# Optimization experiments

Measured on AMD Instinct MI355X. Metric: run time of the kernel, lower is better.

## Reference

```python
import jax, jax.numpy as jnp
import numpy as np

B, O, C, HID, H, W = 4, 8, 256, 128, 64, 64
STEPS = 2  # message passing steps


def _conv3x3(x, w, b):
    # x: [N,Cin,H,W], w: [Cout,Cin,3,3]
    y = jax.lax.conv_general_dilated(x, w, window_strides=(1, 1), padding='SAME',
                                     dimension_numbers=('NCHW', 'OIHW', 'NCHW'))
    return y + b[None, :, None, None]


def setup_inputs() -> dict:
    key = jax.random.key(0)
    ks = jax.random.split(key, 6)
    return {
        'batch_node_feats': jax.random.normal(ks[0], (B, C, H, W), jnp.float32),
        'batch_previous_masks': jax.random.uniform(ks[1], (B, O, H, W), jnp.float32),
        'batch_valid_indices': jnp.ones((B, O), jnp.bool_),
        'batch_previous_states': jnp.zeros((B, O), jnp.float32),  # unused (use_temporal_features=False)
        'enc_w': jax.random.normal(ks[2], (HID, C + 1, 3, 3), jnp.float32) * 0.02,
        'enc_b': jnp.zeros((HID,), jnp.float32),
        'gcn_w': jax.random.normal(ks[3], (HID, 2 * HID, 3, 3), jnp.float32) * 0.02,
        'gcn_b': jnp.zeros((HID,), jnp.float32),
        'ro_w': jax.random.normal(ks[4], (1, C + HID, 3, 3), jnp.float32) * 0.02,
        'ro_b': jnp.zeros((1,), jnp.float32),
    }


def reference(batch_node_feats, batch_previous_masks, batch_valid_indices,
              batch_previous_states, enc_w, enc_b, gcn_w, gcn_b, ro_w, ro_b):
    # All objects valid (batch_valid_indices all True) -> fully vectorized over B and O.
    feats = jnp.broadcast_to(batch_node_feats[:, None], (B, O, C, H, W))
    # Mask encoder: per-object state from frame feats + previous object mask.
    enc_in = jnp.concatenate([feats, batch_previous_masks[:, :, None]], axis=2)
    states = jax.nn.relu(_conv3x3(enc_in.reshape(B * O, C + 1, H, W), enc_w, enc_b))
    states = states.reshape(B, O, HID, H, W)
    # Fully-connected message passing: neighbors of i = all objects except i.
    for _ in range(STEPS):
        agg = states.sum(axis=1, keepdims=True) - states  # sum over others
        gcn_in = jnp.concatenate([states, agg], axis=2).reshape(B * O, 2 * HID, H, W)
        states = jax.nn.relu(_conv3x3(gcn_in, gcn_w, gcn_b)).reshape(B, O, HID, H, W)
    # Readout: per-object mask logits -> sigmoid.
    ro_in = jnp.concatenate([feats, states], axis=2).reshape(B * O, C + HID, H, W)
    out_masks = jax.nn.sigmoid(_conv3x3(ro_in, ro_w, ro_b)).reshape(B, O, H, W)
    return out_masks  # out_states is None when use_temporal_features=False
```

## Files before the change

### kernel.cpp

```cpp
#include <hip/hip_runtime.h>
#include <math.h>


typedef unsigned short ushort_t;
typedef _Float16 f16x8 __attribute__((ext_vector_type(8)));
typedef float f32x4 __attribute__((ext_vector_type(4)));

#define GLDS(gsrc, ldst)                                                      \
    __builtin_amdgcn_global_load_lds(                                         \
        (const __attribute__((address_space(1))) unsigned int*)(gsrc),        \
        (__attribute__((address_space(3))) unsigned int*)(ldst), 16, 0, 0)

__device__ __forceinline__ ushort_t f2h(float f) {
    _Float16 h = (_Float16)f;
    return *(ushort_t*)&h;
}
__device__ __forceinline__ float h2f(ushort_t u) {
    _Float16 h = *(_Float16*)&u;
    return (float)h;
}
__device__ __forceinline__ int swz(int p, int q) {
    return q ^ (((p >> 1) + (p >> 3)) & 3);
}

__global__ __launch_bounds__(256) void prep_weights(
    const float* __restrict__ enc_w, const float* __restrict__ gcn_w,
    const float* __restrict__ ro_w,
    ushort_t* __restrict__ WencF, ushort_t* __restrict__ WgcnS,
    ushort_t* __restrict__ WgcnD, ushort_t* __restrict__ WroQ,
    ushort_t* __restrict__ WroS)
{
    int i = blockIdx.x * 256 + threadIdx.x;
    if (i < 294912) {
        int u8 = i & 7, q = (i >> 3) & 3, co = (i >> 5) & 127, tc = i >> 12;
        int t = tc >> 3, cc = tc & 7;
        int ci = cc * 32 + swz(co & 63, q) * 8 + u8;
        WencF[i] = f2h(enc_w[(co * 257 + ci) * 9 + t]);
    } else if (i < 442368) {
        int j = i - 294912;
        int u8 = j & 7, q = (j >> 3) & 3, co = (j >> 5) & 127, tc = j >> 12;
        int t = tc >> 2, cc = tc & 3;
        int ci = cc * 32 + swz(co & 63, q) * 8 + u8;
        WgcnS[j] = f2h(gcn_w[(co * 256 + 128 + ci) * 9 + t]);
    } else if (i < 589824) {
        int j = i - 442368;
        int u8 = j & 7, q = (j >> 3) & 3, co = (j >> 5) & 127, tc = j >> 12;
        int t = tc >> 2, cc = tc & 3;
        int ci = cc * 32 + swz(co & 63, q) * 8 + u8;
        WgcnD[j] = f2h(gcn_w[(co * 256 + ci) * 9 + t] - gcn_w[(co * 256 + 128 + ci) * 9 + t]);
    } else if (i < 592128) {
        int j = i - 589824;
        int k = j & 7, r = j >> 3;
        int t = r % 9, cq = r / 9, q = cq & 3, cc = cq >> 2;
        WroQ[j] = f2h(ro_w[(cc * 32 + q * 8 + k) * 9 + t]);
    } else if (i < 593280) {
        int j = i - 592128;
        int k = j & 7, r = j >> 3;
        int t = r % 9, cq = r / 9, q = cq & 3, cc = cq >> 2;
        WroS[j] = f2h(ro_w[(256 + cc * 32 + q * 8 + k) * 9 + t]);
    }
}

__global__ __launch_bounds__(256) void feats_to_hwc(const float* __restrict__ feats,
                                                    ushort_t* __restrict__ featsT)
{
    __shared__ float tile[64][65];
    int img = blockIdx.z, ct = blockIdx.y, pt = blockIdx.x;
    int t = threadIdx.x;
    int px_l = t & 63;
    const float* src = feats + ((size_t)img * 256 + ct * 64) * 4096 + pt * 64;
#pragma unroll
    for (int j = 0; j < 16; ++j) {
        int ci_l = (t >> 6) + j * 4;
        tile[px_l][ci_l] = src[(size_t)ci_l * 4096 + px_l];
    }
    __syncthreads();
    int px = t >> 2;
#pragma unroll
    for (int j = 0; j < 2; ++j) {
        int c8 = ((t & 3) + j * 4) * 8;
        uint4 v; ushort_t* pv = (ushort_t*)&v;
#pragma unroll
        for (int k = 0; k < 8; ++k) pv[k] = f2h(tile[px][c8 + k]);
        int cc = ct * 2 + (c8 >> 5);
        int q = (c8 & 31) >> 3;
        *(uint4*)(featsT + ((size_t)img * 8 + cc) * 131072 +
                  (size_t)(pt * 64 + px) * 32 + swz(px, q) * 8) = v;
    }
}

__global__ __launch_bounds__(256, 3) void conv_mfma(
    const ushort_t* __restrict__ xA, const ushort_t* __restrict__ WA,
    ushort_t* __restrict__ outA, int nA,
    const ushort_t* __restrict__ xB, const ushort_t* __restrict__ WB,
    float* __restrict__ outB, int nB,
    int ncc_img, int ncc_blk)
{
    __shared__ ushort_t raw[25088];
    ushort_t* xs = raw;
    ushort_t* wlds = raw + 16896;
    ushort_t* eb16 = raw;
    float* eb32 = (float*)raw;

    const int rp = blockIdx.x, img = blockIdx.y, kz = blockIdx.z;
    const int row0 = rp * 2;
    const int cc0 = kz * ncc_blk;
    const int nchunk = 9 * ncc_blk;
    const int tid = threadIdx.x;
    const int w = tid >> 6, lane = tid & 63, lq = lane >> 4, lr = lane & 15;
    const int cg = w >> 1, pg = w & 1;

    const bool isA = img < nA;
    const ushort_t* x = isA ? xA + (size_t)img * ncc_img * 131072
                            : xB + (size_t)(img - nA) * ncc_img * 131072;
    const ushort_t* W = isA ? WA : WB;

    int aoff[4], boff[3][4];
#pragma unroll
    for (int cf = 0; cf < 4; ++cf) {
        int co = cg * 64 + cf * 16 + lr;
        aoff[cf] = co * 32 + swz(co & 63, lq) * 8;
    }
#pragma unroll
    for (int dx = 0; dx < 3; ++dx)
#pragma unroll
        for (int p = 0; p < 4; ++p) {
            int col = dx + lr + p * 16;
            boff[dx][p] = col * 32 + swz((col - 1) & 63, lq) * 8;
        }

    if (tid < 64) {
        int b = tid >> 5, r = (tid >> 3) & 3, c = (tid >> 2) & 1, s = tid & 3;
        *(uint4*)(xs + b * 8448 + r * 2112 + (c ? 65 : 0) * 32 + s * 8) =
            make_uint4(0, 0, 0, 0);
    }

    f32x4 acc[4][4];
#pragma unroll
    for (int a = 0; a < 4; ++a)
#pragma unroll
        for (int p = 0; p < 4; ++p) acc[a][p] = (f32x4){0.f, 0.f, 0.f, 0.f};

    const int gy = row0 - 1 + w;
    const bool row_ok = (unsigned)gy < 64u;
#define STAGE_ACT(cc_, buf_)                                                    \
    {                                                                           \
        ushort_t* dst = xs + (buf_) * 8448 + w * 2112 + 32;                     \
        if (row_ok) {                                                           \
            const ushort_t* src = x + (size_t)(cc_) * 131072 + (size_t)gy * 2048; \
            GLDS(src + 0 * 512 + lane * 8, dst + 0 * 512);                      \
            GLDS(src + 1 * 512 + lane * 8, dst + 1 * 512);                      \
            GLDS(src + 2 * 512 + lane * 8, dst + 2 * 512);                      \
            GLDS(src + 3 * 512 + lane * 8, dst + 3 * 512);                      \
        } else {                                                                \
            *(uint4*)(dst + 0 * 512 + lane * 8) = make_uint4(0, 0, 0, 0);       \
            *(uint4*)(dst + 1 * 512 + lane * 8) = make_uint4(0, 0, 0, 0);       \
            *(uint4*)(dst + 2 * 512 + lane * 8) = make_uint4(0, 0, 0, 0);       \
            *(uint4*)(dst + 3 * 512 + lane * 8) = make_uint4(0, 0, 0, 0);       \
        }                                                                       \
    }
#define STAGE_W(t_, cc_, buf_)                                                  \
    {                                                                           \
        const ushort_t* src = W + ((size_t)((t_) * ncc_img + (cc_)) * 4096);    \
        ushort_t* dst = wlds + (buf_) * 4096;                                   \
        GLDS(src + (w * 2 + 0) * 512 + lane * 8, dst + (w * 2 + 0) * 512);      \
        GLDS(src + (w * 2 + 1) * 512 + lane * 8, dst + (w * 2 + 1) * 512);      \
    }

    STAGE_ACT(cc0, 0);
    STAGE_W(0, cc0, 0);

    int kc = 0;
    for (int ccl = 0; ccl < ncc_blk; ++ccl) {
        const int cc = cc0 + ccl;
        const int xb = ccl & 1;
#pragma unroll
        for (int t = 0; t < 9; ++t, ++kc) {
            __syncthreads();
            if (kc + 1 < nchunk) {
                if (t == 8) {
                    STAGE_W(0, cc + 1, (kc + 1) & 1);
                    STAGE_ACT(cc + 1, (ccl + 1) & 1);
                } else {
                    STAGE_W(t + 1, cc, (kc + 1) & 1);
                }
            }
            const int dy = t / 3, dx = t - 3 * dy;
            const ushort_t* wl = wlds + (kc & 1) * 4096;
            const ushort_t* xl = xs + xb * 8448 + (pg + dy) * 2112;
            f16x8 A0 = *(const f16x8*)(wl + aoff[0]);
            f16x8 A1 = *(const f16x8*)(wl + aoff[1]);
            f16x8 A2 = *(const f16x8*)(wl + aoff[2]);
            f16x8 A3 = *(const f16x8*)(wl + aoff[3]);
#pragma unroll
            for (int p = 0; p < 4; ++p) {
                f16x8 Bf = *(const f16x8*)(xl + boff[dx][p]);
                acc[0][p] = __builtin_amdgcn_mfma_f32_16x16x32_f16(A0, Bf, acc[0][p], 0, 0, 0);
                acc[1][p] = __builtin_amdgcn_mfma_f32_16x16x32_f16(A1, Bf, acc[1][p], 0, 0, 0);
                acc[2][p] = __builtin_amdgcn_mfma_f32_16x16x32_f16(A2, Bf, acc[2][p], 0, 0, 0);
                acc[3][p] = __builtin_amdgcn_mfma_f32_16x16x32_f16(A3, Bf, acc[3][p], 0, 0, 0);
            }
        }
    }

    if (isA) {
        ushort_t* obase = outA + (size_t)img * ncc_img * 131072;
#pragma unroll
        for (int r = 0; r < 2; ++r) {
            __syncthreads();
            if (pg == r) {
#pragma unroll
                for (int cf = 0; cf < 4; ++cf)
#pragma unroll
                    for (int pf = 0; pf < 4; ++pf) {
                        int px = pf * 16 + lr;
                        int co_l = cg * 64 + cf * 16 + lq * 4;
                        ushort_t pk[4];
#pragma unroll
                        for (int j = 0; j < 4; ++j) pk[j] = f2h(acc[cf][pf][j]);
                        *(uint2*)(eb16 + px * 136 + co_l) = *(uint2*)pk;
                    }
            }
            __syncthreads();
#pragma unroll
            for (int k = 0; k < 4; ++k) {
                int i = tid + k * 256;
                int px = i >> 4, c16 = i & 15;
                uint4 v = *(uint4*)(eb16 + px * 136 + c16 * 8);
                *(uint4*)(obase + (size_t)(c16 >> 2) * 131072 +
                          (size_t)((row0 + r) * 64 + px) * 32 + swz(px, c16 & 3) * 8) = v;
            }
        }
    } else {
        float* obase = outB + ((size_t)kz * nB + (img - nA)) * 524288;
#pragma unroll
        for (int r = 0; r < 2; ++r)
#pragma unroll
            for (int h = 0; h < 2; ++h) {
                __syncthreads();
                if (pg == r && cg == h) {
#pragma unroll
                    for (int cf = 0; cf < 4; ++cf)
#pragma unroll
                        for (int pf = 0; pf < 4; ++pf)
                            *(f32x4*)(eb32 + (pf * 16 + lr) * 68 + cf * 16 + lq * 4) =
                                acc[cf][pf];
                }
                __syncthreads();
                for (int i = tid; i < 512; i += 256) {
                    int px = i >> 3, cl = (i & 7) * 8;
                    f32x4 v0 = *(f32x4*)(eb32 + px * 68 + cl);
                    f32x4 v1 = *(f32x4*)(eb32 + px * 68 + cl + 4);
                    float* op = obase + (size_t)((row0 + r) * 64 + px) * 128 + h * 64 + cl;
                    *(f32x4*)op = v0;
                    *(f32x4*)(op + 4) = v1;
                }
            }
    }
#undef STAGE_ACT
#undef STAGE_W
}

__global__ __launch_bounds__(256) void combine_sum(
    ushort_t* __restrict__ S, const float* __restrict__ U2,
    const float* __restrict__ gcn_b, ushort_t* __restrict__ USum)
{
    int i = blockIdx.x * 256 + threadIdx.x;
    int c8 = i & 15, px = (i >> 4) & 4095, b = i >> 16;
    int co = c8 * 8;
    size_t coff = (size_t)(c8 >> 2) * 131072 + (size_t)px * 32 + swz(px & 63, c8 & 3) * 8;
    const float* u = U2 + ((size_t)b * 4096 + px) * 128 + co;
    float base[8];
#pragma unroll
    for (int k = 0; k < 8; ++k) base[k] = u[k] + gcn_b[co + k];
    float s[8] = {0, 0, 0, 0, 0, 0, 0, 0};
#pragma unroll
    for (int o = 0; o < 8; ++o) {
        ushort_t* p = S + (size_t)(b * 8 + o) * 524288 + coff;
        uint4 v = *(uint4*)p;
        ushort_t* vp = (ushort_t*)&v;
        uint4 sv; ushort_t* sp = (ushort_t*)&sv;
#pragma unroll
        for (int k = 0; k < 8; ++k) {
            float f = fmaxf(h2f(vp[k]) + base[k], 0.f);
            s[k] += f;
            sp[k] = f2h(f);
        }
        *(uint4*)p = sv;
    }
    uint4 sv; ushort_t* sp = (ushort_t*)&sv;
#pragma unroll
    for (int k = 0; k < 8; ++k) sp[k] = f2h(s[k]);
    *(uint4*)(USum + (size_t)b * 524288 + coff) = sv;
}

__global__ __launch_bounds__(256) void enc_obj_sum(
    const float* __restrict__ masks, const float* __restrict__ enc_w,
    const float* __restrict__ enc_b, const float* __restrict__ U1p,
    ushort_t* __restrict__ S, ushort_t* __restrict__ USum)
{
    int i = blockIdx.x * 256 + threadIdx.x;
    int c8 = i & 15, px = (i >> 4) & 4095, b = i >> 16;
    int co = c8 * 8;
    int y = px >> 6, xx = px & 63;
    size_t coff = (size_t)(c8 >> 2) * 131072 + (size_t)px * 32 + swz(px & 63, c8 & 3) * 8;
    const float* p0 = U1p + ((size_t)b * 4096 + px) * 128 + co;
    float base[8];
#pragma unroll
    for (int k = 0; k < 8; ++k)
        base[k] = ((p0[k] + p0[k + 2097152]) + (p0[k + 4194304] + p0[k + 6291456]))
                  + enc_b[co + k];
    float wm[8][9];
#pragma unroll
    for (int k = 0; k < 8; ++k) {
        const float* wp = enc_w + (size_t)((co + k) * 257 + 256) * 9;
#pragma unroll
        for (int t = 0; t < 9; ++t) wm[k][t] = wp[t];
    }
    float s[8] = {0, 0, 0, 0, 0, 0, 0, 0};
#pragma unroll
    for (int o = 0; o < 8; ++o) {
        const float* m = masks + (size_t)(b * 8 + o) * 4096;
        float mt[9];
#pragma unroll
        for (int dy = 0; dy < 3; ++dy)
#pragma unroll
            for (int dx = 0; dx < 3; ++dx) {
                int gy_ = y + dy - 1, gx = xx + dx - 1;
                mt[dy * 3 + dx] =
                    ((unsigned)gy_ < 64u && (unsigned)gx < 64u) ? m[gy_ * 64 + gx] : 0.f;
            }
        uint4 sv; ushort_t* sp = (ushort_t*)&sv;
#pragma unroll
        for (int k = 0; k < 8; ++k) {
            float acc = base[k];
#pragma unroll
            for (int t = 0; t < 9; ++t) acc = fmaf(mt[t], wm[k][t], acc);
            acc = fmaxf(acc, 0.f);
            s[k] += acc;
            sp[k] = f2h(acc);
        }
        *(uint4*)(S + (size_t)(b * 8 + o) * 524288 + coff) = sv;
    }
    uint4 sv; ushort_t* sp = (ushort_t*)&sv;
#pragma unroll
    for (int k = 0; k < 8; ++k) sp[k] = f2h(s[k]);
    *(uint4*)(USum + (size_t)b * 524288 + coff) = sv;
}

__global__ __launch_bounds__(256) void ro_shared(
    const ushort_t* __restrict__ featsT, const ushort_t* __restrict__ WroQ,
    float* __restrict__ YR)
{
    int i = blockIdx.x * 256 + threadIdx.x;
    int cu = i & 31, px = (i >> 5) & 4095, b = i >> 17;
    int cc = cu >> 2, q = cu & 3;
    int y = px >> 6, xcol = px & 63;
    const ushort_t* wp = WroQ + (size_t)(cc * 4 + q) * 72;
    float wreg[9][8];
#pragma unroll
    for (int t = 0; t < 9; ++t) {
        uint4 wv = *(const uint4*)(wp + t * 8);
        const ushort_t* wq = (const ushort_t*)&wv;
#pragma unroll
        for (int k = 0; k < 8; ++k) wreg[t][k] = h2f(wq[k]);
    }
    const ushort_t* fb = featsT + (size_t)(b * 8 + cc) * 131072;
    float acc = 0.f;
#pragma unroll
    for (int dy = 0; dy < 3; ++dy) {
        int gy = y + dy - 1;
        if ((unsigned)gy >= 64u) continue;
#pragma unroll
        for (int dx = 0; dx < 3; ++dx) {
            int gx = xcol + dx - 1;
            if ((unsigned)gx >= 64u) continue;
            uint4 v = *(const uint4*)(fb + (size_t)(gy * 64 + gx) * 32 + swz(gx, q) * 8);
            const ushort_t* vp = (const ushort_t*)&v;
#pragma unroll
            for (int k = 0; k < 8; ++k)
                acc = fmaf(h2f(vp[k]), wreg[dy * 3 + dx][k], acc);
        }
    }
#pragma unroll
    for (int d = 16; d >= 1; d >>= 1) acc += __shfl_down(acc, d, 32);
    if (cu == 0) YR[b * 4096 + px] = acc;
}

__global__ __launch_bounds__(256) void ro_obj(
    const ushort_t* __restrict__ S, const ushort_t* __restrict__ WroS,
    const float* __restrict__ ro_b, const float* __restrict__ YR,
    float* __restrict__ out)
{
    int i = blockIdx.x * 256 + threadIdx.x;
    int cu = i & 15, px = (i >> 4) & 4095, n = i >> 16;
    int b = n >> 3;
    int cc = cu >> 2, q = cu & 3;
    int y = px >> 6, xcol = px & 63;
    const ushort_t* wp = WroS + (size_t)(cc * 4 + q) * 72;
    float wreg[9][8];
#pragma unroll
    for (int t = 0; t < 9; ++t) {
        uint4 wv = *(const uint4*)(wp + t * 8);
        const ushort_t* wq = (const ushort_t*)&wv;
#pragma unroll
        for (int k = 0; k < 8; ++k) wreg[t][k] = h2f(wq[k]);
    }
    const ushort_t* sb = S + ((size_t)n * 4 + cc) * 131072;
    float acc = 0.f;
#pragma unroll
    for (int dy = 0; dy < 3; ++dy) {
        int gy = y + dy - 1;
        if ((unsigned)gy >= 64u) continue;
#pragma unroll
        for (int dx = 0; dx < 3; ++dx) {
            int gx = xcol + dx - 1;
            if ((unsigned)gx >= 64u) continue;
            uint4 v = *(const uint4*)(sb + (size_t)(gy * 64 + gx) * 32 + swz(gx, q) * 8);
            const ushort_t* vp = (const ushort_t*)&v;
#pragma unroll
            for (int k = 0; k < 8; ++k)
                acc = fmaf(h2f(vp[k]), wreg[dy * 3 + dx][k], acc);
        }
    }
#pragma unroll
    for (int d = 8; d >= 1; d >>= 1) acc += __shfl_down(acc, d, 16);
    if (cu == 0) {
        float v = acc + YR[b * 4096 + px] + ro_b[0];
        out[n * 4096 + px] = 1.f / (1.f + __expf(-v));
    }
}

extern "C" void kernel_launch(void* const* d_in, const int* in_sizes, int n_in,
                              void* d_out, int out_size, void* d_ws, size_t ws_size,
                              hipStream_t stream)
{
    const float* feats = (const float*)d_in[0];
    const float* masks = (const float*)d_in[1];
    const float* enc_w = (const float*)d_in[4];
    const float* enc_b = (const float*)d_in[5];
    const float* gcn_w = (const float*)d_in[6];
    const float* gcn_b = (const float*)d_in[7];
    const float* ro_w  = (const float*)d_in[8];
    const float* ro_b  = (const float*)d_in[9];
    float* out = (float*)d_out;

    ushort_t* WencF  = (ushort_t*)d_ws;
    ushort_t* WgcnS  = WencF + 294912;
    ushort_t* WgcnD  = WgcnS + 147456;
    ushort_t* WroQ   = WgcnD + 147456;
    ushort_t* WroS   = WroQ + 2304;
    ushort_t* featsT = WroS + 1152;
    ushort_t* Sa     = featsT + 4194304;
    ushort_t* Sb     = Sa + 16777216;
    ushort_t* USum   = Sb + 16777216;
    float*    U1p    = (float*)(USum + 2097152);
    float*    U2     = U1p + 8388608;
    float*    YR     = U2 + 2097152;

    dim3 blk(256);

    prep_weights<<<2320, blk, 0, stream>>>(enc_w, gcn_w, ro_w,
                                           WencF, WgcnS, WgcnD, WroQ, WroS);
    feats_to_hwc<<<dim3(64, 4, 4), blk, 0, stream>>>(feats, featsT);

    conv_mfma<<<dim3(32, 4, 4), blk, 0, stream>>>(
        nullptr, nullptr, nullptr, 0, featsT, WencF, U1p, 4, 8, 2);
    enc_obj_sum<<<1024, blk, 0, stream>>>(masks, enc_w, enc_b, U1p, Sa, USum);

    conv_mfma<<<dim3(32, 36, 1), blk, 0, stream>>>(
        Sa, WgcnD, Sb, 32, USum, WgcnS, U2, 4, 4, 4);
    combine_sum<<<1024, blk, 0, stream>>>(Sb, U2, gcn_b, USum);

    conv_mfma<<<dim3(32, 36, 1), blk, 0, stream>>>(
        Sb, WgcnD, Sa, 32, USum, WgcnS, U2, 4, 4, 4);
    combine_sum<<<1024, blk, 0, stream>>>(Sa, U2, gcn_b, USum);

    ro_shared<<<2048, blk, 0, stream>>>(featsT, WroQ, YR);
    ro_obj<<<8192, blk, 0, stream>>>(Sa, WroS, ro_b, YR, out);
}
```

Measured before the change: 274.3 us.

## Stage three filter taps per barrier and drop LDS swizzle in conv pipeline

The MFMA conv kernel now loads weights for a full row of three taps (dx) per stage instead of one tap, so there are three barriers per channel chunk instead of nine. The activation buffer becomes single-buffered and is reloaded behind an extra barrier. The XOR swizzle on the channel-within-pixel layout is removed everywhere, from weight prep through the elementwise and readout kernels. Occupancy drops from 3 to 2 blocks per CU because of the larger LDS footprint. Removing the swizzle risks LDS bank conflicts on the B-fragment reads, and the activation reload is no longer overlapped with compute.

```diff
diff --git a/kernel.cpp b/kernel.cpp
--- a/kernel.cpp
+++ b/kernel.cpp
@@ -18,9 +18,6 @@
 __device__ __forceinline__ float h2f(ushort_t u) {
     _Float16 h = *(_Float16*)&u;
     return (float)h;
-}
-__device__ __forceinline__ int swz(int p, int q) {
-    return q ^ (((p >> 1) + (p >> 3)) & 3);
 }
 
 __global__ __launch_bounds__(256) void prep_weights(
@@ -32,21 +29,18 @@
 {
     int i = blockIdx.x * 256 + threadIdx.x;
     if (i < 294912) {
-        int u8 = i & 7, q = (i >> 3) & 3, co = (i >> 5) & 127, tc = i >> 12;
-        int t = tc >> 3, cc = tc & 7;
-        int ci = cc * 32 + swz(co & 63, q) * 8 + u8;
+        int ci32 = i & 31, co = (i >> 5) & 127, tc = i >> 12;
+        int t = tc >> 3, cc = tc & 7, ci = cc * 32 + ci32;
         WencF[i] = f2h(enc_w[(co * 257 + ci) * 9 + t]);
     } else if (i < 442368) {
         int j = i - 294912;
-        int u8 = j & 7, q = (j >> 3) & 3, co = (j >> 5) & 127, tc = j >> 12;
-        int t = tc >> 2, cc = tc & 3;
-        int ci = cc * 32 + swz(co & 63, q) * 8 + u8;
+        int ci32 = j & 31, co = (j >> 5) & 127, tc = j >> 12;
+        int t = tc >> 2, cc = tc & 3, ci = cc * 32 + ci32;
         WgcnS[j] = f2h(gcn_w[(co * 256 + 128 + ci) * 9 + t]);
     } else if (i < 589824) {
         int j = i - 442368;
-        int u8 = j & 7, q = (j >> 3) & 3, co = (j >> 5) & 127, tc = j >> 12;
-        int t = tc >> 2, cc = tc & 3;
-        int ci = cc * 32 + swz(co & 63, q) * 8 + u8;
+        int ci32 = j & 31, co = (j >> 5) & 127, tc = j >> 12;
+        int t = tc >> 2, cc = tc & 3, ci = cc * 32 + ci32;
         WgcnD[j] = f2h(gcn_w[(co * 256 + ci) * 9 + t] - gcn_w[(co * 256 + 128 + ci) * 9 + t]);
     } else if (i < 592128) {
         int j = i - 589824;
@@ -83,29 +77,27 @@
 #pragma unroll
         for (int k = 0; k < 8; ++k) pv[k] = f2h(tile[px][c8 + k]);
         int cc = ct * 2 + (c8 >> 5);
-        int q = (c8 & 31) >> 3;
         *(uint4*)(featsT + ((size_t)img * 8 + cc) * 131072 +
-                  (size_t)(pt * 64 + px) * 32 + swz(px, q) * 8) = v;
-    }
-}
-
-__global__ __launch_bounds__(256, 3) void conv_mfma(
+                  (size_t)(pt * 64 + px) * 32 + (c8 & 31)) = v;
+    }
+}
+
+__global__ __launch_bounds__(256, 2) void conv_mfma(
     const ushort_t* __restrict__ xA, const ushort_t* __restrict__ WA,
     ushort_t* __restrict__ outA, int nA,
     const ushort_t* __restrict__ xB, const ushort_t* __restrict__ WB,
     float* __restrict__ outB, int nB,
     int ncc_img, int ncc_blk)
 {
-    __shared__ ushort_t raw[25088];
+    __shared__ ushort_t raw[33024];
     ushort_t* xs = raw;
-    ushort_t* wlds = raw + 16896;
+    ushort_t* wlds = raw + 8448;
     ushort_t* eb16 = raw;
     float* eb32 = (float*)raw;
 
     const int rp = blockIdx.x, img = blockIdx.y, kz = blockIdx.z;
     const int row0 = rp * 2;
     const int cc0 = kz * ncc_blk;
-    const int nchunk = 9 * ncc_blk;
     const int tid = threadIdx.x;
     const int w = tid >> 6, lane = tid & 63, lq = lane >> 4, lr = lane & 15;
     const int cg = w >> 1, pg = w & 1;
@@ -115,24 +107,11 @@
                             : xB + (size_t)(img - nA) * ncc_img * 131072;
     const ushort_t* W = isA ? WA : WB;
 
-    int aoff[4], boff[3][4];
-#pragma unroll
-    for (int cf = 0; cf < 4; ++cf) {
-        int co = cg * 64 + cf * 16 + lr;
-        aoff[cf] = co * 32 + swz(co & 63, lq) * 8;
-    }
-#pragma unroll
-    for (int dx = 0; dx < 3; ++dx)
-#pragma unroll
-        for (int p = 0; p < 4; ++p) {
-            int col = dx + lr + p * 16;
-            boff[dx][p] = col * 32 + swz((col - 1) & 63, lq) * 8;
-        }
-
-    if (tid < 64) {
-        int b = tid >> 5, r = (tid >> 3) & 3, c = (tid >> 2) & 1, s = tid & 3;
-        *(uint4*)(xs + b * 8448 + r * 2112 + (c ? 65 : 0) * 32 + s * 8) =
-            make_uint4(0, 0, 0, 0);
+    const int aoff0 = (cg * 64 + lr) * 32 + lq * 8;
+
+    if (tid < 32) {
+        int r = tid >> 3, c = (tid >> 2) & 1, s = tid & 3;
+        *(uint4*)(xs + r * 2112 + (c ? 65 : 0) * 32 + s * 8) = make_uint4(0, 0, 0, 0);
     }
 
     f32x4 acc[4][4];
@@ -143,63 +122,72 @@
 
     const int gy = row0 - 1 + w;
     const bool row_ok = (unsigned)gy < 64u;
-#define STAGE_ACT(cc_, buf_)                                                    \
+
+#define STAGE_ACT(cc_)                                                          \
     {                                                                           \
-        ushort_t* dst = xs + (buf_) * 8448 + w * 2112 + 32;                     \
+        ushort_t* adst = xs + w * 2112 + 32;                                    \
         if (row_ok) {                                                           \
-            const ushort_t* src = x + (size_t)(cc_) * 131072 + (size_t)gy * 2048; \
-            GLDS(src + 0 * 512 + lane * 8, dst + 0 * 512);                      \
-            GLDS(src + 1 * 512 + lane * 8, dst + 1 * 512);                      \
-            GLDS(src + 2 * 512 + lane * 8, dst + 2 * 512);                      \
-            GLDS(src + 3 * 512 + lane * 8, dst + 3 * 512);                      \
+            const ushort_t* asrc =                                              \
+                x + (size_t)(cc_) * 131072 + (size_t)gy * 2048 + lane * 8;      \
+            GLDS(asrc + 0 * 512, adst + 0 * 512);                               \
+            GLDS(asrc + 1 * 512, adst + 1 * 512);                               \
+            GLDS(asrc + 2 * 512, adst + 2 * 512);                               \
+            GLDS(asrc + 3 * 512, adst + 3 * 512);                               \
         } else {                                                                \
-            *(uint4*)(dst + 0 * 512 + lane * 8) = make_uint4(0, 0, 0, 0);       \
-            *(uint4*)(dst + 1 * 512 + lane * 8) = make_uint4(0, 0, 0, 0);       \
-            *(uint4*)(dst + 2 * 512 + lane * 8) = make_uint4(0, 0, 0, 0);       \
-            *(uint4*)(dst + 3 * 512 + lane * 8) = make_uint4(0, 0, 0, 0);       \
+            *(uint4*)(adst + 0 * 512 + lane * 8) = make_uint4(0, 0, 0, 0);      \
+            *(uint4*)(adst + 1 * 512 + lane * 8) = make_uint4(0, 0, 0, 0);      \
+            *(uint4*)(adst + 2 * 512 + lane * 8) = make_uint4(0, 0, 0, 0);      \
+            *(uint4*)(adst + 3 * 512 + lane * 8) = make_uint4(0, 0, 0, 0);      \
         }                                                                       \
     }
-#define STAGE_W(t_, cc_, buf_)                                                  \
+#define STAGE_W(t0_, cc_, buf_)                                                 \
     {                                                                           \
-        const ushort_t* src = W + ((size_t)((t_) * ncc_img + (cc_)) * 4096);    \
-        ushort_t* dst = wlds + (buf_) * 4096;                                   \
-        GLDS(src + (w * 2 + 0) * 512 + lane * 8, dst + (w * 2 + 0) * 512);      \
-        GLDS(src + (w * 2 + 1) * 512 + lane * 8, dst + (w * 2 + 1) * 512);      \
-    }
-
-    STAGE_ACT(cc0, 0);
+        ushort_t* wdst = wlds + (buf_) * 12288;                                 \
+        _Pragma("unroll")                                                       \
+        for (int r_ = w * 6; r_ < w * 6 + 6; ++r_) {                            \
+            int g_ = r_ >> 3, rem_ = (r_ & 7) * 512;                            \
+            GLDS(W + ((size_t)((t0_) + g_) * ncc_img + (cc_)) * 4096 + rem_ +   \
+                     lane * 8,                                                  \
+                 wdst + g_ * 4096 + rem_);                                      \
+        }                                                                       \
+    }
+
+    STAGE_ACT(cc0);
     STAGE_W(0, cc0, 0);
 
-    int kc = 0;
     for (int ccl = 0; ccl < ncc_blk; ++ccl) {
         const int cc = cc0 + ccl;
-        const int xb = ccl & 1;
-#pragma unroll
-        for (int t = 0; t < 9; ++t, ++kc) {
+#pragma unroll
+        for (int g = 0; g < 3; ++g) {
             __syncthreads();
-            if (kc + 1 < nchunk) {
-                if (t == 8) {
-                    STAGE_W(0, cc + 1, (kc + 1) & 1);
-                    STAGE_ACT(cc + 1, (ccl + 1) & 1);
-                } else {
-                    STAGE_W(t + 1, cc, (kc + 1) & 1);
+            const int par = (ccl + g) & 1;
+            if (g < 2) {
+                STAGE_W(3 * (g + 1), cc, par ^ 1);
+            } else if (ccl + 1 < ncc_blk) {
+                STAGE_W(0, cc + 1, par ^ 1);
+            }
+            const ushort_t* wb = wlds + par * 12288;
+            const ushort_t* xrow = xs + (pg + g) * 2112 + lq * 8;
+#pragma unroll
+            for (int dx = 0; dx < 3; ++dx) {
+                const ushort_t* wt = wb + dx * 4096 + aoff0;
+                f16x8 A0 = *(const f16x8*)(wt);
+                f16x8 A1 = *(const f16x8*)(wt + 512);
+                f16x8 A2 = *(const f16x8*)(wt + 1024);
+                f16x8 A3 = *(const f16x8*)(wt + 1536);
+#pragma unroll
+                for (int p = 0; p < 4; ++p) {
+                    f16x8 Bf = *(const f16x8*)(xrow + (dx + lr + p * 16) * 32);
+                    acc[0][p] = __builtin_amdgcn_mfma_f32_16x16x32_f16(A0, Bf, acc[0][p], 0, 0, 0);
+                    acc[1][p] = __builtin_amdgcn_mfma_f32_16x16x32_f16(A1, Bf, acc[1][p], 0, 0, 0);
+                    acc[2][p] = __builtin_amdgcn_mfma_f32_16x16x32_f16(A2, Bf, acc[2][p], 0, 0, 0);
+                    acc[3][p] = __builtin_amdgcn_mfma_f32_16x16x32_f16(A3, Bf, acc[3][p], 0, 0, 0);
                 }
             }
-            const int dy = t / 3, dx = t - 3 * dy;
-            const ushort_t* wl = wlds + (kc & 1) * 4096;
-            const ushort_t* xl = xs + xb * 8448 + (pg + dy) * 2112;
-            f16x8 A0 = *(const f16x8*)(wl + aoff[0]);
-            f16x8 A1 = *(const f16x8*)(wl + aoff[1]);
-            f16x8 A2 = *(const f16x8*)(wl + aoff[2]);
-            f16x8 A3 = *(const f16x8*)(wl + aoff[3]);
-#pragma unroll
-            for (int p = 0; p < 4; ++p) {
-                f16x8 Bf = *(const f16x8*)(xl + boff[dx][p]);
-                acc[0][p] = __builtin_amdgcn_mfma_f32_16x16x32_f16(A0, Bf, acc[0][p], 0, 0, 0);
-                acc[1][p] = __builtin_amdgcn_mfma_f32_16x16x32_f16(A1, Bf, acc[1][p], 0, 0, 0);
-                acc[2][p] = __builtin_amdgcn_mfma_f32_16x16x32_f16(A2, Bf, acc[2][p], 0, 0, 0);
-                acc[3][p] = __builtin_amdgcn_mfma_f32_16x16x32_f16(A3, Bf, acc[3][p], 0, 0, 0);
-            }
+        }
+        if (ccl + 1 < ncc_blk) {
+            __syncthreads();
+            STAGE_ACT(cc + 1);
         }
     }
 
@@ -228,7 +216,7 @@
                 int px = i >> 4, c16 = i & 15;
                 uint4 v = *(uint4*)(eb16 + px * 136 + c16 * 8);
                 *(uint4*)(obase + (size_t)(c16 >> 2) * 131072 +
-                          (size_t)((row0 + r) * 64 + px) * 32 + swz(px, c16 & 3) * 8) = v;
+                          (size_t)((row0 + r) * 64 + px) * 32 + (c16 & 3) * 8) = v;
             }
         }
     } else {
@@ -268,7 +256,7 @@
     int i = blockIdx.x * 256 + threadIdx.x;
     int c8 = i & 15, px = (i >> 4) & 4095, b = i >> 16;
     int co = c8 * 8;
-    size_t coff = (size_t)(c8 >> 2) * 131072 + (size_t)px * 32 + swz(px & 63, c8 & 3) * 8;
+    size_t coff = (size_t)(c8 >> 2) * 131072 + (size_t)px * 32 + (c8 & 3) * 8;
     const float* u = U2 + ((size_t)b * 4096 + px) * 128 + co;
     float base[8];
 #pragma unroll
@@ -303,7 +291,7 @@
     int c8 = i & 15, px = (i >> 4) & 4095, b = i >> 16;
     int co = c8 * 8;
     int y = px >> 6, xx = px & 63;
-    size_t coff = (size_t)(c8 >> 2) * 131072 + (size_t)px * 32 + swz(px & 63, c8 & 3) * 8;
+    size_t coff = (size_t)(c8 >> 2) * 131072 + (size_t)px * 32 + (c8 & 3) * 8;
     const float* p0 = U1p + ((size_t)b * 4096 + px) * 128 + co;
     float base[8];
 #pragma unroll
@@ -365,7 +353,7 @@
 #pragma unroll
         for (int k = 0; k < 8; ++k) wreg[t][k] = h2f(wq[k]);
     }
-    const ushort_t* fb = featsT + (size_t)(b * 8 + cc) * 131072;
+    const ushort_t* fb = featsT + (size_t)(b * 8 + cc) * 131072 + q * 8;
     float acc = 0.f;
 #pragma unroll
     for (int dy = 0; dy < 3; ++dy) {
@@ -375,7 +363,7 @@
         for (int dx = 0; dx < 3; ++dx) {
             int gx = xcol + dx - 1;
             if ((unsigned)gx >= 64u) continue;
-            uint4 v = *(const uint4*)(fb + (size_t)(gy * 64 + gx) * 32 + swz(gx, q) * 8);
+            uint4 v = *(const uint4*)(fb + (size_t)(gy * 64 + gx) * 32);
             const ushort_t* vp = (const ushort_t*)&v;
 #pragma unroll
             for (int k = 0; k < 8; ++k)
@@ -406,7 +394,7 @@
 #pragma unroll
         for (int k = 0; k < 8; ++k) wreg[t][k] = h2f(wq[k]);
     }
-    const ushort_t* sb = S + ((size_t)n * 4 + cc) * 131072;
+    const ushort_t* sb = S + ((size_t)n * 4 + cc) * 131072 + q * 8;
     float acc = 0.f;
 #pragma unroll
     for (int dy = 0; dy < 3; ++dy) {
@@ -416,7 +404,7 @@
         for (int dx = 0; dx < 3; ++dx) {
             int gx = xcol + dx - 1;
             if ((unsigned)gx >= 64u) continue;
-            uint4 v = *(const uint4*)(sb + (size_t)(gy * 64 + gx) * 32 + swz(gx, q) * 8);
+            uint4 v = *(const uint4*)(sb + (size_t)(gy * 64 + gx) * 32);
             const ushort_t* vp = (const ushort_t*)&v;
 #pragma unroll
             for (int k = 0; k < 8; ++k)
```

New measurement: 272.8 us. Within noise of the previous version (-0.5%).

## Drop LDS swizzle and split encoder conv K eight ways with fp16 partials

Applied to the files above, without the earlier changes.

Removes the XOR swizzle from the HWC activation and weight layouts, so every LDS and global index becomes a plain linear offset and the precomputed per-lane offset tables go away. The encoder convolution is now split into eight channel-chunk slices, each writing fp16 partial outputs through the A path, and enc_obj_sum adds the eight partials. This gives the encoder conv more blocks in flight and trims index arithmetic and registers. The cost is likely LDS bank conflicts on the MFMA operand reads without the swizzle, plus lower precision from storing partial sums in fp16.

```diff
diff --git a/kernel.cpp b/kernel.cpp
--- a/kernel.cpp
+++ b/kernel.cpp
@@ -18,9 +18,6 @@
 __device__ __forceinline__ float h2f(ushort_t u) {
     _Float16 h = *(_Float16*)&u;
     return (float)h;
-}
-__device__ __forceinline__ int swz(int p, int q) {
-    return q ^ (((p >> 1) + (p >> 3)) & 3);
 }
 
 __global__ __launch_bounds__(256) void prep_weights(
@@ -32,21 +29,18 @@
 {
     int i = blockIdx.x * 256 + threadIdx.x;
     if (i < 294912) {
-        int u8 = i & 7, q = (i >> 3) & 3, co = (i >> 5) & 127, tc = i >> 12;
-        int t = tc >> 3, cc = tc & 7;
-        int ci = cc * 32 + swz(co & 63, q) * 8 + u8;
+        int ci32 = i & 31, co = (i >> 5) & 127, tc = i >> 12;
+        int t = tc >> 3, cc = tc & 7, ci = cc * 32 + ci32;
         WencF[i] = f2h(enc_w[(co * 257 + ci) * 9 + t]);
     } else if (i < 442368) {
         int j = i - 294912;
-        int u8 = j & 7, q = (j >> 3) & 3, co = (j >> 5) & 127, tc = j >> 12;
-        int t = tc >> 2, cc = tc & 3;
-        int ci = cc * 32 + swz(co & 63, q) * 8 + u8;
+        int ci32 = j & 31, co = (j >> 5) & 127, tc = j >> 12;
+        int t = tc >> 2, cc = tc & 3, ci = cc * 32 + ci32;
         WgcnS[j] = f2h(gcn_w[(co * 256 + 128 + ci) * 9 + t]);
     } else if (i < 589824) {
         int j = i - 442368;
-        int u8 = j & 7, q = (j >> 3) & 3, co = (j >> 5) & 127, tc = j >> 12;
-        int t = tc >> 2, cc = tc & 3;
-        int ci = cc * 32 + swz(co & 63, q) * 8 + u8;
+        int ci32 = j & 31, co = (j >> 5) & 127, tc = j >> 12;
+        int t = tc >> 2, cc = tc & 3, ci = cc * 32 + ci32;
         WgcnD[j] = f2h(gcn_w[(co * 256 + ci) * 9 + t] - gcn_w[(co * 256 + 128 + ci) * 9 + t]);
     } else if (i < 592128) {
         int j = i - 589824;
@@ -83,9 +77,8 @@
 #pragma unroll
         for (int k = 0; k < 8; ++k) pv[k] = f2h(tile[px][c8 + k]);
         int cc = ct * 2 + (c8 >> 5);
-        int q = (c8 & 31) >> 3;
         *(uint4*)(featsT + ((size_t)img * 8 + cc) * 131072 +
-                  (size_t)(pt * 64 + px) * 32 + swz(px, q) * 8) = v;
+                  (size_t)(pt * 64 + px) * 32 + (c8 & 31)) = v;
     }
 }
 
@@ -115,19 +108,7 @@
                             : xB + (size_t)(img - nA) * ncc_img * 131072;
     const ushort_t* W = isA ? WA : WB;
 
-    int aoff[4], boff[3][4];
-#pragma unroll
-    for (int cf = 0; cf < 4; ++cf) {
-        int co = cg * 64 + cf * 16 + lr;
-        aoff[cf] = co * 32 + swz(co & 63, lq) * 8;
-    }
-#pragma unroll
-    for (int dx = 0; dx < 3; ++dx)
-#pragma unroll
-        for (int p = 0; p < 4; ++p) {
-            int col = dx + lr + p * 16;
-            boff[dx][p] = col * 32 + swz((col - 1) & 63, lq) * 8;
-        }
+    const int aoff0 = (cg * 64 + lr) * 32 + lq * 8;
 
     if (tid < 64) {
         int b = tid >> 5, r = (tid >> 3) & 3, c = (tid >> 2) & 1, s = tid & 3;
@@ -186,15 +167,15 @@
                 }
             }
             const int dy = t / 3, dx = t - 3 * dy;
-            const ushort_t* wl = wlds + (kc & 1) * 4096;
-            const ushort_t* xl = xs + xb * 8448 + (pg + dy) * 2112;
-            f16x8 A0 = *(const f16x8*)(wl + aoff[0]);
-            f16x8 A1 = *(const f16x8*)(wl + aoff[1]);
-            f16x8 A2 = *(const f16x8*)(wl + aoff[2]);
-            f16x8 A3 = *(const f16x8*)(wl + aoff[3]);
+            const ushort_t* wl = wlds + (kc & 1) * 4096 + aoff0;
+            const ushort_t* xl = xs + xb * 8448 + (pg + dy) * 2112 + (dx + lr) * 32 + lq * 8;
+            f16x8 A0 = *(const f16x8*)(wl);
+            f16x8 A1 = *(const f16x8*)(wl + 512);
+            f16x8 A2 = *(const f16x8*)(wl + 1024);
+            f16x8 A3 = *(const f16x8*)(wl + 1536);
 #pragma unroll
             for (int p = 0; p < 4; ++p) {
-                f16x8 Bf = *(const f16x8*)(xl + boff[dx][p]);
+                f16x8 Bf = *(const f16x8*)(xl + p * 512);
                 acc[0][p] = __builtin_amdgcn_mfma_f32_16x16x32_f16(A0, Bf, acc[0][p], 0, 0, 0);
                 acc[1][p] = __builtin_amdgcn_mfma_f32_16x16x32_f16(A1, Bf, acc[1][p], 0, 0, 0);
                 acc[2][p] = __builtin_amdgcn_mfma_f32_16x16x32_f16(A2, Bf, acc[2][p], 0, 0, 0);
@@ -204,7 +185,7 @@
     }
 
     if (isA) {
-        ushort_t* obase = outA + (size_t)img * ncc_img * 131072;
+        ushort_t* obase = outA + (size_t)(kz * nA + img) * 524288;
 #pragma unroll
         for (int r = 0; r < 2; ++r) {
             __syncthreads();
@@ -228,7 +209,7 @@
                 int px = i >> 4, c16 = i & 15;
                 uint4 v = *(uint4*)(eb16 + px * 136 + c16 * 8);
                 *(uint4*)(obase + (size_t)(c16 >> 2) * 131072 +
-                          (size_t)((row0 + r) * 64 + px) * 32 + swz(px, c16 & 3) * 8) = v;
+                          (size_t)((row0 + r) * 64 + px) * 32 + (c16 & 3) * 8) = v;
             }
         }
     } else {
@@ -268,7 +249,7 @@
     int i = blockIdx.x * 256 + threadIdx.x;
     int c8 = i & 15, px = (i >> 4) & 4095, b = i >> 16;
     int co = c8 * 8;
-    size_t coff = (size_t)(c8 >> 2) * 131072 + (size_t)px * 32 + swz(px & 63, c8 & 3) * 8;
+    size_t coff = (size_t)(c8 >> 2) * 131072 + (size_t)px * 32 + (c8 & 3) * 8;
     const float* u = U2 + ((size_t)b * 4096 + px) * 128 + co;
     float base[8];
 #pragma unroll
@@ -296,20 +277,24 @@
 
 __global__ __launch_bounds__(256) void enc_obj_sum(
     const float* __restrict__ masks, const float* __restrict__ enc_w,
-    const float* __restrict__ enc_b, const float* __restrict__ U1p,
+    const float* __restrict__ enc_b, const ushort_t* __restrict__ U1p,
     ushort_t* __restrict__ S, ushort_t* __restrict__ USum)
 {
     int i = blockIdx.x * 256 + threadIdx.x;
     int c8 = i & 15, px = (i >> 4) & 4095, b = i >> 16;
     int co = c8 * 8;
     int y = px >> 6, xx = px & 63;
-    size_t coff = (size_t)(c8 >> 2) * 131072 + (size_t)px * 32 + swz(px & 63, c8 & 3) * 8;
-    const float* p0 = U1p + ((size_t)b * 4096 + px) * 128 + co;
+    size_t coff = (size_t)(c8 >> 2) * 131072 + (size_t)px * 32 + (c8 & 3) * 8;
     float base[8];
 #pragma unroll
-    for (int k = 0; k < 8; ++k)
-        base[k] = ((p0[k] + p0[k + 2097152]) + (p0[k + 4194304] + p0[k + 6291456]))
-                  + enc_b[co + k];
+    for (int k = 0; k < 8; ++k) base[k] = enc_b[co + k];
+#pragma unroll
+    for (int p = 0; p < 8; ++p) {
+        uint4 v = *(const uint4*)(U1p + (size_t)(p * 4 + b) * 524288 + coff);
+        const ushort_t* vp = (const ushort_t*)&v;
+#pragma unroll
+        for (int k = 0; k < 8; ++k) base[k] += h2f(vp[k]);
+    }
     float wm[8][9];
 #pragma unroll
     for (int k = 0; k < 8; ++k) {
@@ -365,7 +350,7 @@
 #pragma unroll
         for (int k = 0; k < 8; ++k) wreg[t][k] = h2f(wq[k]);
     }
-    const ushort_t* fb = featsT + (size_t)(b * 8 + cc) * 131072;
+    const ushort_t* fb = featsT + (size_t)(b * 8 + cc) * 131072 + q * 8;
     float acc = 0.f;
 #pragma unroll
     for (int dy = 0; dy < 3; ++dy) {
@@ -375,7 +360,7 @@
         for (int dx = 0; dx < 3; ++dx) {
             int gx = xcol + dx - 1;
             if ((unsigned)gx >= 64u) continue;
-            uint4 v = *(const uint4*)(fb + (size_t)(gy * 64 + gx) * 32 + swz(gx, q) * 8);
+            uint4 v = *(const uint4*)(fb + (size_t)(gy * 64 + gx) * 32);
             const ushort_t* vp = (const ushort_t*)&v;
 #pragma unroll
             for (int k = 0; k < 8; ++k)
@@ -406,7 +391,7 @@
 #pragma unroll
         for (int k = 0; k < 8; ++k) wreg[t][k] = h2f(wq[k]);
     }
-    const ushort_t* sb = S + ((size_t)n * 4 + cc) * 131072;
+    const ushort_t* sb = S + ((size_t)n * 4 + cc) * 131072 + q * 8;
     float acc = 0.f;
 #pragma unroll
     for (int dy = 0; dy < 3; ++dy) {
@@ -416,7 +401,7 @@
         for (int dx = 0; dx < 3; ++dx) {
             int gx = xcol + dx - 1;
             if ((unsigned)gx >= 64u) continue;
-            uint4 v = *(const uint4*)(sb + (size_t)(gy * 64 + gx) * 32 + swz(gx, q) * 8);
+            uint4 v = *(const uint4*)(sb + (size_t)(gy * 64 + gx) * 32);
             const ushort_t* vp = (const ushort_t*)&v;
 #pragma unroll
             for (int k = 0; k < 8; ++k)
@@ -454,8 +439,8 @@
     ushort_t* Sa     = featsT + 4194304;
     ushort_t* Sb     = Sa + 16777216;
     ushort_t* USum   = Sb + 16777216;
-    float*    U1p    = (float*)(USum + 2097152);
-    float*    U2     = U1p + 8388608;
+    ushort_t* U1p16  = USum + 2097152;
+    float*    U2     = (float*)(U1p16 + 16777216);
     float*    YR     = U2 + 2097152;
 
     dim3 blk(256);
@@ -464,9 +449,9 @@
                                            WencF, WgcnS, WgcnD, WroQ, WroS);
     feats_to_hwc<<<dim3(64, 4, 4), blk, 0, stream>>>(feats, featsT);
 
-    conv_mfma<<<dim3(32, 4, 4), blk, 0, stream>>>(
-        nullptr, nullptr, nullptr, 0, featsT, WencF, U1p, 4, 8, 2);
-    enc_obj_sum<<<1024, blk, 0, stream>>>(masks, enc_w, enc_b, U1p, Sa, USum);
+    conv_mfma<<<dim3(32, 4, 8), blk, 0, stream>>>(
+        featsT, WencF, U1p16, 4, nullptr, nullptr, nullptr, 0, 8, 1);
+    enc_obj_sum<<<1024, blk, 0, stream>>>(masks, enc_w, enc_b, U1p16, Sa, USum);
 
     conv_mfma<<<dim3(32, 36, 1), blk, 0, stream>>>(
         Sa, WgcnD, Sb, 32, USum, WgcnS, U2, 4, 4, 4);
```

New measurement: 272.1 us. No clear change (-0.8%).
